# Optimization experiments

Hardware: AMD Instinct MI355X
Metric: run time of the kernel (lower is better)

The kernel has to match this reference:

```python
import math
import jax, jax.numpy as jnp
import numpy as np

DIM = 1024
FFN_DIM = 4096
NUM_HEADS = 16
HEAD_DIM = DIM // NUM_HEADS
SCALE = 1.0 / math.sqrt(HEAD_DIM)
EPS = 1e-5


def _layer_norm(x, gamma, beta):
    mu = jnp.mean(x, axis=-1, keepdims=True)
    var = jnp.mean(jnp.square(x - mu), axis=-1, keepdims=True)
    return (x - mu) * jax.lax.rsqrt(var + EPS) * gamma + beta


def _gelu_erf(x):
    # matches torch GELU module: x * 0.5 * (1 + erf(x / sqrt(2)))
    return x * 0.5 * (1.0 + jax.lax.erf(x / math.sqrt(2.0)))


def setup_inputs() -> dict:
    key = jax.random.key(0)
    ks = jax.random.split(key, 12)
    B, L = 2, 2048
    s = 0.02
    inp = {
        "x": jax.random.normal(ks[0], (B, L, DIM), dtype=jnp.float32),
        "g1": jnp.ones((DIM,), jnp.float32),
        "b1": jnp.zeros((DIM,), jnp.float32),
        "Wq": jax.random.normal(ks[1], (DIM, DIM), jnp.float32) * s,
        "bq": jnp.zeros((DIM,), jnp.float32),
        "Wk": jax.random.normal(ks[2], (DIM, DIM), jnp.float32) * s,
        "bk": jnp.zeros((DIM,), jnp.float32),
        "Wv": jax.random.normal(ks[3], (DIM, DIM), jnp.float32) * s,
        "bv": jnp.zeros((DIM,), jnp.float32),
        "Wo": jax.random.normal(ks[4], (DIM, DIM), jnp.float32) * s,
        "bo": jnp.zeros((DIM,), jnp.float32),
        "g2": jnp.ones((DIM,), jnp.float32),
        "b2": jnp.zeros((DIM,), jnp.float32),
        "W1": jax.random.normal(ks[5], (FFN_DIM, DIM), jnp.float32) * s,
        "bf1": jnp.zeros((FFN_DIM,), jnp.float32),
        "W2": jax.random.normal(ks[6], (DIM, FFN_DIM), jnp.float32) * s,
        "bf2": jnp.zeros((DIM,), jnp.float32),
    }
    return inp


def reference(x, g1, b1, Wq, bq, Wk, bk, Wv, bv, Wo, bo, g2, b2, W1, bf1, W2, bf2):
    B, L, C = x.shape
    n, c = NUM_HEADS, HEAD_DIM

    # ---- pre-norm self-attention ----
    h = _layer_norm(x, g1, b1)
    q = (h @ Wq.T + bq).reshape(B, L, n, c)
    k = (h @ Wk.T + bk).reshape(B, L, n, c)
    v = (h @ Wv.T + bv).reshape(B, L, n, c)
    attn = SCALE * jnp.einsum('binc,bjnc->bnij', q, k)   # [B, n, L, L]
    attn = jax.nn.softmax(attn, axis=-1)
    o = jnp.einsum('bnij,bjnc->binc', attn, v).reshape(B, L, C)
    x = x + (o @ Wo.T + bo)

    # ---- pre-norm FFN (GELU, erf form) ----
    h = _layer_norm(x, g2, b2)
    h = _gelu_erf(h @ W1.T + bf1)
    x = x + (h @ W2.T + bf2)
    return x
```

## Files before the change

kernel.cpp:

```cpp
#include <hip/hip_runtime.h>
#include <hip/hip_bf16.h>
#include <math.h>

typedef unsigned short u16;
typedef __attribute__((ext_vector_type(8))) __bf16 bf16x8;
typedef __attribute__((ext_vector_type(4))) float f32x4;

#define DIM   1024
#define LSEQ  2048
#define BTOK  4096
#define HD    64
#define FFN   4096
#define QSCL  0.18033688011112042f

#if __has_builtin(__builtin_amdgcn_exp2f)
#define EXP2(x) __builtin_amdgcn_exp2f(x)
#else
#define EXP2(x) exp2f(x)
#endif

__device__ __forceinline__ u16 f2bf(float f) {
  unsigned u = __builtin_bit_cast(unsigned, f);
  u += 0x7FFFu + ((u >> 16) & 1u);
  return (u16)(u >> 16);
}
__device__ __forceinline__ unsigned pk2(float a, float b) {
  return (unsigned)f2bf(a) | ((unsigned)f2bf(b) << 16);
}
__device__ __forceinline__ unsigned cvtpk(float lo, float hi) {
  unsigned r;
  asm("v_cvt_pk_bf16_f32 %0, %1, %2" : "=v"(r) : "v"(lo), "v"(hi));
  return r;
}
__device__ __forceinline__ f32x4 mfma16(bf16x8 a, bf16x8 b, f32x4 c) {
  return __builtin_amdgcn_mfma_f32_16x16x32_bf16(a, b, c, 0, 0, 0);
}
__device__ __forceinline__ void gload16(const void* g, void* l) {
  __builtin_amdgcn_global_load_lds((const __attribute__((address_space(1))) char*)g,
                                   (__attribute__((address_space(3))) char*)l, 16, 0, 0);
}
__device__ __forceinline__ float gelu_t(float v) {
  float v3 = v * v * v;
  float tt = fmaf(-0.10296766f, v3, -2.30258509f * v);
  return v * __builtin_amdgcn_rcpf(1.0f + EXP2(tt));
}

__global__ __launch_bounds__(256) void ln_kernel(const float* __restrict__ x,
                                                 const float* __restrict__ g,
                                                 const float* __restrict__ bta,
                                                 u16* __restrict__ out) {
  int row = blockIdx.x, t = threadIdx.x;
  const float* xr = x + (size_t)row * DIM;
  float4 xv = *(const float4*)(xr + t * 4);
  float s  = xv.x + xv.y + xv.z + xv.w;
  float ss = xv.x * xv.x + xv.y * xv.y + xv.z * xv.z + xv.w * xv.w;
#pragma unroll
  for (int m = 32; m >= 1; m >>= 1) {
    s  += __shfl_xor(s, m);
    ss += __shfl_xor(ss, m);
  }
  __shared__ float red[8];
  if ((t & 63) == 0) { red[(t >> 6) * 2] = s; red[(t >> 6) * 2 + 1] = ss; }
  __syncthreads();
  s  = red[0] + red[2] + red[4] + red[6];
  ss = red[1] + red[3] + red[5] + red[7];
  float mu  = s * (1.0f / DIM);
  float var = ss * (1.0f / DIM) - mu * mu;
  float rs  = rsqrtf(var + 1e-5f);
  float4 gv = *(const float4*)(g + t * 4);
  float4 bv = *(const float4*)(bta + t * 4);
  uint2 o;
  o.x = pk2((xv.x - mu) * rs * gv.x + bv.x, (xv.y - mu) * rs * gv.y + bv.y);
  o.y = pk2((xv.z - mu) * rs * gv.z + bv.z, (xv.w - mu) * rs * gv.w + bv.w);
  *(uint2*)(out + (size_t)row * DIM + t * 4) = o;
}

__global__ __launch_bounds__(256) void wcvt4(const float* __restrict__ Wq, const float* __restrict__ Wk,
                                             const float* __restrict__ Wv, const float* __restrict__ Wo,
                                             u16* __restrict__ dst) {
  int b = blockIdx.x;
  int r = b >> 9;
  const float* s = (r == 0) ? Wq : (r == 1) ? Wk : (r == 2) ? Wv : Wo;
  size_t i = (((size_t)(b & 511)) * 256 + threadIdx.x) * 8;
  float4 f0 = *(const float4*)(s + i), f1 = *(const float4*)(s + i + 4);
  uint4 o = { pk2(f0.x, f0.y), pk2(f0.z, f0.w), pk2(f1.x, f1.y), pk2(f1.z, f1.w) };
  *(uint4*)(dst + ((size_t)r << 20) + i) = o;
}
__global__ __launch_bounds__(256) void wcvt2(const float* __restrict__ W1, const float* __restrict__ W2,
                                             u16* __restrict__ d1, u16* __restrict__ d2) {
  int b = blockIdx.x;
  const float* s = (b < 2048) ? W1 : W2;
  u16* d = (b < 2048) ? d1 : d2;
  size_t i = (((size_t)(b & 2047)) * 256 + threadIdx.x) * 8;
  float4 f0 = *(const float4*)(s + i), f1 = *(const float4*)(s + i + 4);
  uint4 o = { pk2(f0.x, f0.y), pk2(f0.z, f0.w), pk2(f1.x, f1.y), pk2(f1.z, f1.w) };
  *(uint4*)(d + i) = o;
}

__global__ __launch_bounds__(256) void transpose_v(const u16* __restrict__ v,
                                                   u16* __restrict__ vt) {
  __shared__ u16 tls[64][80];
  int jb = blockIdx.x, bh = blockIdx.y, b = bh >> 4, h = bh & 15;
  int t = threadIdx.x;
  int r = t >> 2, seg = t & 3;
  const u16* src = v + (size_t)(b * LSEQ + jb * 64 + r) * DIM + h * HD + seg * 16;
  *(uint4*)&tls[r][seg * 16]     = *(const uint4*)src;
  *(uint4*)&tls[r][seg * 16 + 8] = *(const uint4*)(src + 8);
  __syncthreads();
  int c = t >> 2, jseg = t & 3;
  u16 tmp[16] __attribute__((aligned(16)));
#pragma unroll
  for (int i = 0; i < 16; i++) tmp[i] = tls[jseg * 16 + i][c];
  u16* dst = vt + ((size_t)bh * HD + c) * LSEQ + jb * 64 + jseg * 16;
  *(uint4*)dst       = *(const uint4*)tmp;
  *(uint4*)(dst + 8) = *(const uint4*)(tmp + 8);
}

__global__ __launch_bounds__(256) void prefill(float* __restrict__ io,
                                               const float* __restrict__ a,
                                               const float* __restrict__ bias) {
  size_t i = ((size_t)blockIdx.x * 256 + threadIdx.x) * 4;
  float4 va = *(const float4*)(a + i);
  float4 vc = *(const float4*)(bias + (i & (DIM - 1)));
  va.x += vc.x; va.y += vc.y; va.z += vc.z; va.w += vc.w;
  *(float4*)(io + i) = va;
}

struct GArg { const u16* Wb; const float* bias; u16* outB; float oscale; };

template <int EPI, int BM, int DEPTH>
__global__ __launch_bounds__(256) void gemm4(const u16* __restrict__ A,
                                             GArg g0, GArg g1, GArg g2,
                                             float* __restrict__ outF,
                                             int N, int Kstride, int Kiter, int nbPerW) {
  constexpr int WM  = BM / 32;
  constexpr int LPT = BM / 64 + 2;
  constexpr int ABUF = BM * 64;
  constexpr int BBUF = 8192;
  constexpr int VX  = (DEPTH - 2) * LPT;
  __shared__ u16 lsa[DEPTH][BM * 32];
  __shared__ u16 lsb[DEPTH][128 * 32];
  const int t = threadIdx.x;
  const int w = t >> 6, l = t & 63, l15 = l & 15, lg = l >> 4;
  const int wr = w >> 1, wc = w & 1;
  const int nwg = gridDim.x * gridDim.y;
  int flat = blockIdx.y * gridDim.x + blockIdx.x;
  flat = (flat & 7) * (nwg >> 3) + (flat >> 3);
  const int bx = flat % gridDim.x, by = flat / gridDim.x;
  const int sel = bx / nbPerW, nb = bx % nbPerW;
  GArg G = (sel == 0) ? g0 : ((sel == 1) ? g1 : g2);
  const int n0 = nb * 128, m0 = by * BM;
  const int z = blockIdx.z;
  const int koff = z * Kiter;

  f32x4 acc[WM][4];
#pragma unroll
  for (int m = 0; m < WM; m++)
#pragma unroll
    for (int n = 0; n < 4; n++) acc[m][n] = (f32x4){0.f, 0.f, 0.f, 0.f};

  const int grow = t >> 2;
  const int gcol = 8 * ((t & 3) ^ ((t >> 3) & 3));
  const u16* Asrc = A + (size_t)(m0 + grow) * Kstride + koff + gcol;
  const u16* Bsrc = G.Wb + (size_t)(n0 + grow) * Kstride + koff + gcol;
  const int rs = (l15 >> 1) & 3;

  const char* aadr = (const char*)lsa + (wr * (BM / 2) + l15) * 64 + (lg ^ rs) * 16;
  const char* badr = (const char*)lsb + (wc * 64 + l15) * 64 + (lg ^ rs) * 16;

  auto stage = [&](int k0, int buf) {
#pragma unroll
    for (int i = 0; i < BM / 64; i++)
      gload16(Asrc + (size_t)i * 64 * Kstride + k0, (char*)lsa + buf * ABUF + i * 4096 + w * 1024);
#pragma unroll
    for (int i = 0; i < 2; i++)
      gload16(Bsrc + (size_t)i * 64 * Kstride + k0, (char*)lsb + buf * BBUF + i * 4096 + w * 1024);
  };

#pragma unroll
  for (int p = 0; p < DEPTH - 1; p++) stage(p << 5, p);

  const int NT = Kiter >> 5;
  int bufR = 0, bufW = DEPTH - 1;
  for (int it = 0; it < NT; it++) {
    if (it + 1 < NT) {
      if constexpr (VX == 3)      asm volatile("s_waitcnt vmcnt(3)" ::: "memory");
      else if constexpr (VX == 4) asm volatile("s_waitcnt vmcnt(4)" ::: "memory");
      else if constexpr (VX == 6) asm volatile("s_waitcnt vmcnt(6)" ::: "memory");
      else                        asm volatile("s_waitcnt vmcnt(0)" ::: "memory");
    } else {
      asm volatile("s_waitcnt vmcnt(0)" ::: "memory");
    }
    __builtin_amdgcn_s_barrier();
    asm volatile("" ::: "memory");

    if (it + DEPTH - 1 < NT) stage((it + DEPTH - 1) << 5, bufW);

    const char* ap = aadr + bufR * ABUF;
    const char* bp = badr + bufR * BBUF;
    bf16x8 af[WM], bfr[4];
#pragma unroll
    for (int m = 0; m < WM; m++)
      af[m] = *(const bf16x8*)(ap + m * 1024);
#pragma unroll
    for (int n = 0; n < 4; n++)
      bfr[n] = *(const bf16x8*)(bp + n * 1024);
    __builtin_amdgcn_s_setprio(1);
#pragma unroll
    for (int m = 0; m < WM; m++)
#pragma unroll
      for (int n = 0; n < 4; n++)
        acc[m][n] = mfma16(af[m], bfr[n], acc[m][n]);
    __builtin_amdgcn_s_setprio(0);
    bufR = (bufR + 1 == DEPTH) ? 0 : bufR + 1;
    bufW = (bufW + 1 == DEPTH) ? 0 : bufW + 1;
  }

#pragma unroll
  for (int m = 0; m < WM; m++) {
    const int row = m0 + wr * (BM / 2) + m * 16 + lg * 4;
#pragma unroll
    for (int n = 0; n < 4; n++) {
      const int col = n0 + wc * 64 + n * 16 + l15;
      float bcol;
      if (EPI == 4) bcol = (z == 0 && G.bias != nullptr) ? G.bias[col] : 0.f;
      else          bcol = G.bias[col];
#pragma unroll
      for (int r = 0; r < 4; r++) {
        const float v = acc[m][n][r] + bcol;
        const size_t idx = (size_t)(row + r) * N + col;
        if (EPI == 0)      G.outB[idx] = f2bf(v * G.oscale);
        else if (EPI == 4) atomicAdd(&outF[idx], v);
        else               G.outB[idx] = f2bf(gelu_t(v));
      }
    }
  }
}

__global__ __launch_bounds__(256, 4) void attn5(const u16* __restrict__ q,
                                                const u16* __restrict__ k,
                                                const u16* __restrict__ vt,
                                                u16* __restrict__ o) {
  __shared__ __align__(16) char smem[40960];
  const int t = threadIdx.x, w = t >> 6, l = t & 63, l15 = l & 15, lg = l >> 4;
  int flat = blockIdx.y * gridDim.x + blockIdx.x;
  flat = (flat & 7) * 128 + (flat >> 3);
  const int qbk = flat & 31, bh = flat >> 5;
  const int b = bh >> 4, h = bh & 15;
  const int qrow0 = b * LSEQ + qbk * 64 + w * 16;
  const int r7 = l15 & 7;
  const int c0 = lg ^ r7;

  bf16x8 av[2];
#pragma unroll
  for (int i = 0; i < 2; i++)
    av[i] = *(const bf16x8*)(q + (size_t)(qrow0 + l15) * DIM + h * HD + i * 32 + lg * 8);

  const char* adrA  = smem + l15 * 128 + c0 * 16;
  const char* adrB  = smem + l15 * 128 + (c0 ^ 4) * 16;
  const char* padrA = smem + 32768 + w * 2048 + l15 * 128 + c0 * 16;
  const char* padrB = smem + 32768 + w * 2048 + l15 * 128 + (c0 ^ 4) * 16;
  char* pwa[4];
#pragma unroll
  for (int cb = 0; cb < 4; cb++)
    pwa[cb] = smem + 32768 + w * 2048 + l15 * 128 +
              (((2 * cb + (lg >> 1)) ^ r7) * 16) + (lg & 1) * 8;

  const int grow = t >> 3, gchk = t & 7;
  const u16* ksrc = k + (size_t)(b * LSEQ + grow) * DIM + h * HD + 8 * (gchk ^ (grow & 7));
  const u16* vsrc = vt + ((size_t)bh * HD + grow) * LSEQ + 8 * (gchk ^ (grow & 7));

  f32x4 oacc[4];
#pragma unroll
  for (int cb = 0; cb < 4; cb++) oacc[cb] = (f32x4){0.f, 0.f, 0.f, 0.f};
  f32x4 minit = (f32x4){0.f, 0.f, 0.f, 0.f};
  float lsum = 0.f;

  auto issueTile = [&](int jt, int buf) {
    const u16* kp = ksrc + (size_t)jt * DIM;
    const u16* vp = vsrc + jt;
#pragma unroll
    for (int i = 0; i < 2; i++) {
      gload16(kp + (size_t)i * 32 * DIM,  smem + buf * 8192 + i * 4096 + w * 1024);
      gload16(vp + (size_t)i * 32 * LSEQ, smem + 16384 + buf * 8192 + i * 4096 + w * 1024);
    }
  };

  issueTile(0, 0);
  for (int it = 0; it < LSEQ / 64; it++) {
    const int buf = it & 1;
    __syncthreads();
    if (it + 1 < LSEQ / 64) issueTile((it + 1) * 64, buf ^ 1);
    const int ko = buf * 8192;

    f32x4 s[4];
    const char* kA = adrA + ko;
    const char* kB = adrB + ko;
    __builtin_amdgcn_s_setprio(1);
#pragma unroll
    for (int cb = 0; cb < 4; cb++) {
      bf16x8 kf0 = *(const bf16x8*)(kA + cb * 2048);
      bf16x8 kf1 = *(const bf16x8*)(kB + cb * 2048);
      s[cb] = mfma16(kf0, av[0], minit);
      s[cb] = mfma16(kf1, av[1], s[cb]);
    }
    __builtin_amdgcn_s_setprio(0);

    float tm = fmaxf(fmaxf(fmaxf(s[0][0], s[0][1]), fmaxf(s[0][2], s[0][3])),
                     fmaxf(fmaxf(fmaxf(s[1][0], s[1][1]), fmaxf(s[1][2], s[1][3])),
                           fmaxf(fmaxf(fmaxf(s[2][0], s[2][1]), fmaxf(s[2][2], s[2][3])),
                                 fmaxf(fmaxf(s[3][0], s[3][1]), fmaxf(s[3][2], s[3][3])))));
    if (__any(tm > 8.0f)) {
      float tr = fmaxf(tm, __shfl_xor(tm, 16));
      tr = fmaxf(tr, __shfl_xor(tr, 32));
      const float d = fmaxf(tr, 0.f);
      const float scl = EXP2(-d);
      const f32x4 dv = (f32x4){d, d, d, d};
      lsum *= scl;
      minit -= dv;
#pragma unroll
      for (int cb = 0; cb < 4; cb++) s[cb] -= dv;
#pragma unroll
      for (int r = 0; r < 4; r++) {
        const float so = __shfl(scl, lg * 4 + r);
#pragma unroll
        for (int cb = 0; cb < 4; cb++) oacc[cb][r] *= so;
      }
    }
    float ps = 0.f;
    uint2 pk[4];
#pragma unroll
    for (int cb = 0; cb < 4; cb++) {
      float a0 = EXP2(s[cb][0]);
      float a1 = EXP2(s[cb][1]);
      float a2 = EXP2(s[cb][2]);
      float a3 = EXP2(s[cb][3]);
      ps += (a0 + a1) + (a2 + a3);
      pk[cb].x = cvtpk(a0, a1);
      pk[cb].y = cvtpk(a2, a3);
    }
    lsum += ps;
#pragma unroll
    for (int cb = 0; cb < 4; cb++) *(uint2*)pwa[cb] = pk[cb];

    const char* vA = adrA + ko + 16384;
    const char* vB = adrB + ko + 16384;
    bf16x8 pa0 = *(const bf16x8*)padrA;
    bf16x8 pa1 = *(const bf16x8*)padrB;
    __builtin_amdgcn_s_setprio(1);
#pragma unroll
    for (int cb = 0; cb < 4; cb++) {
      bf16x8 vf0 = *(const bf16x8*)(vA + cb * 2048);
      oacc[cb] = mfma16(pa0, vf0, oacc[cb]);
    }
#pragma unroll
    for (int cb = 0; cb < 4; cb++) {
      bf16x8 vf1 = *(const bf16x8*)(vB + cb * 2048);
      oacc[cb] = mfma16(pa1, vf1, oacc[cb]);
    }
    __builtin_amdgcn_s_setprio(0);
  }

  float rl = lsum + __shfl_xor(lsum, 16);
  rl += __shfl_xor(rl, 32);
#pragma unroll
  for (int r = 0; r < 4; r++) {
    const float lo = __shfl(rl, lg * 4 + r);
    const float rcp = 1.0f / lo;
#pragma unroll
    for (int cb = 0; cb < 4; cb++) {
      o[(size_t)(qrow0 + lg * 4 + r) * DIM + h * HD + cb * 16 + l15] =
          f2bf(oacc[cb][r] * rcp);
    }
  }
}

extern "C" void kernel_launch(void* const* d_in, const int* in_sizes, int n_in,
                              void* d_out, int out_size, void* d_ws, size_t ws_size,
                              hipStream_t stream) {
  const float* x   = (const float*)d_in[0];
  const float* g1  = (const float*)d_in[1];
  const float* b1  = (const float*)d_in[2];
  const float* Wq  = (const float*)d_in[3];
  const float* bq  = (const float*)d_in[4];
  const float* Wk  = (const float*)d_in[5];
  const float* bk  = (const float*)d_in[6];
  const float* Wv  = (const float*)d_in[7];
  const float* bv  = (const float*)d_in[8];
  const float* Wo  = (const float*)d_in[9];
  const float* bo  = (const float*)d_in[10];
  const float* g2  = (const float*)d_in[11];
  const float* b2  = (const float*)d_in[12];
  const float* W1  = (const float*)d_in[13];
  const float* bf1 = (const float*)d_in[14];
  const float* W2  = (const float*)d_in[15];
  const float* bf2 = (const float*)d_in[16];
  float* out = (float*)d_out;

  const size_t E = (size_t)BTOK * DIM;
  u16* h     = (u16*)d_ws;
  u16* qb    = h + E;
  u16* kbuf  = qb + E;
  u16* vbuf  = kbuf + E;
  u16* vtb   = vbuf + E;
  u16* wqkvo = vtb + E;
  u16* ob    = vbuf;
  u16* W1b   = qb;
  u16* W2b   = kbuf;
  u16* mid   = vbuf;
  u16* h2    = h;
  float* x2  = out;

  u16* Wqb = wqkvo;
  u16* Wkb = wqkvo + ((size_t)1 << 20);
  u16* Wvb = wqkvo + ((size_t)2 << 20);
  u16* Wob = wqkvo + ((size_t)3 << 20);

  wcvt4<<<dim3(2048), dim3(256), 0, stream>>>(Wq, Wk, Wv, Wo, wqkvo);
  ln_kernel<<<dim3(BTOK), dim3(256), 0, stream>>>(x, g1, b1, h);
  gemm4<0, 128, 3><<<dim3(24, BTOK / 128), 256, 0, stream>>>(
      h, GArg{Wqb, bq, qb, QSCL}, GArg{Wkb, bk, kbuf, 1.0f}, GArg{Wvb, bv, vbuf, 1.0f},
      nullptr, DIM, DIM, DIM, 8);
  transpose_v<<<dim3(32, 32), 256, 0, stream>>>(vbuf, vtb);
  attn5<<<dim3(LSEQ / 64, 32), 256, 0, stream>>>(qb, kbuf, vtb, ob);
  prefill<<<dim3(4096), dim3(256), 0, stream>>>(out, x, bo);
  {
    GArg s{Wob, nullptr, nullptr, 1.0f};
    gemm4<4, 128, 3><<<dim3(8, BTOK / 128, 2), 256, 0, stream>>>(
        ob, s, s, s, out, DIM, DIM, 512, 8);
  }
  wcvt2<<<dim3(4096), dim3(256), 0, stream>>>(W1, W2, W1b, W2b);
  ln_kernel<<<dim3(BTOK), dim3(256), 0, stream>>>(x2, g2, b2, h2);
  {
    GArg s{W1b, bf1, mid, 1.0f};
    gemm4<2, 128, 3><<<dim3(32, BTOK / 128), 256, 0, stream>>>(
        h2, s, s, s, nullptr, FFN, DIM, DIM, 32);
  }
  {
    GArg s{W2b, bf2, nullptr, 1.0f};
    gemm4<4, 128, 3><<<dim3(8, BTOK / 128, 2), 256, 0, stream>>>(
        mid, s, s, s, out, DIM, FFN, 2048, 8);
  }
}
```

Baseline: 285.7 us.

## Replace 128x128 GEMM with 256x256 tile, 512-thread, 4-stage kernel

Swaps the 256-thread 128x128 GEMM for a 512-thread kernel with 256x256 output tiles, 8 waves laid out 2x4, and a 4-deep LDS pipeline. Each wave now computes 128x64. All four GEMM launches move to the new kernel, and the split-K factor for the output and FFN2 projections rises from 2 to 4. The larger tile roughly doubles reuse per byte loaded and halves global traffic per flop. In exchange, LDS rises to 128 KB per block, grids shrink (e.g. 192 blocks for the QKV projection), and split-K adds more fp32 atomic traffic, which may hurt occupancy or load balance.

```diff
diff --git a/kernel.cpp b/kernel.cpp
--- a/kernel.cpp
+++ b/kernel.cpp
@@ -128,53 +128,50 @@
 
 struct GArg { const u16* Wb; const float* bias; u16* outB; float oscale; };
 
-template <int EPI, int BM, int DEPTH>
-__global__ __launch_bounds__(256) void gemm4(const u16* __restrict__ A,
-                                             GArg g0, GArg g1, GArg g2,
-                                             float* __restrict__ outF,
-                                             int N, int Kstride, int Kiter, int nbPerW) {
-  constexpr int WM  = BM / 32;
-  constexpr int LPT = BM / 64 + 2;
-  constexpr int ABUF = BM * 64;
-  constexpr int BBUF = 8192;
-  constexpr int VX  = (DEPTH - 2) * LPT;
-  __shared__ u16 lsa[DEPTH][BM * 32];
-  __shared__ u16 lsb[DEPTH][128 * 32];
+template <int EPI, int DEPTH>
+__global__ __launch_bounds__(512, 2) void gemm8(const u16* __restrict__ A,
+                                                GArg g0, GArg g1, GArg g2,
+                                                float* __restrict__ outF,
+                                                int N, int Kstride, int Kiter, int nbPerW) {
+  constexpr int BUFB = 16384;
+  constexpr int VX   = (DEPTH - 2) * 4;
+  __shared__ u16 lsa[DEPTH][256 * 32];
+  __shared__ u16 lsb[DEPTH][256 * 32];
   const int t = threadIdx.x;
   const int w = t >> 6, l = t & 63, l15 = l & 15, lg = l >> 4;
-  const int wr = w >> 1, wc = w & 1;
+  const int wr = w >> 2, wc = w & 3;
   const int nwg = gridDim.x * gridDim.y;
   int flat = blockIdx.y * gridDim.x + blockIdx.x;
   flat = (flat & 7) * (nwg >> 3) + (flat >> 3);
   const int bx = flat % gridDim.x, by = flat / gridDim.x;
   const int sel = bx / nbPerW, nb = bx % nbPerW;
   GArg G = (sel == 0) ? g0 : ((sel == 1) ? g1 : g2);
-  const int n0 = nb * 128, m0 = by * BM;
+  const int n0 = nb * 256, m0 = by * 256;
   const int z = blockIdx.z;
   const int koff = z * Kiter;
 
-  f32x4 acc[WM][4];
-#pragma unroll
-  for (int m = 0; m < WM; m++)
+  f32x4 acc[8][4];
+#pragma unroll
+  for (int m = 0; m < 8; m++)
 #pragma unroll
     for (int n = 0; n < 4; n++) acc[m][n] = (f32x4){0.f, 0.f, 0.f, 0.f};
 
-  const int grow = t >> 2;
-  const int gcol = 8 * ((t & 3) ^ ((t >> 3) & 3));
-  const u16* Asrc = A + (size_t)(m0 + grow) * Kstride + koff + gcol;
-  const u16* Bsrc = G.Wb + (size_t)(n0 + grow) * Kstride + koff + gcol;
+  const int srow = l >> 2;
+  const int scol = 8 * ((l & 3) ^ ((l >> 3) & 3));
+  const u16* AsrcT = A    + (size_t)(m0 + w * 32 + srow) * Kstride + koff + scol;
+  const u16* BsrcT = G.Wb + (size_t)(n0 + w * 32 + srow) * Kstride + koff + scol;
+
   const int rs = (l15 >> 1) & 3;
-
-  const char* aadr = (const char*)lsa + (wr * (BM / 2) + l15) * 64 + (lg ^ rs) * 16;
-  const char* badr = (const char*)lsb + (wc * 64 + l15) * 64 + (lg ^ rs) * 16;
+  const char* aadr = (const char*)lsa + (wr * 128 + l15) * 64 + ((lg ^ rs) * 16);
+  const char* badr = (const char*)lsb + (wc * 64  + l15) * 64 + ((lg ^ rs) * 16);
 
   auto stage = [&](int k0, int buf) {
 #pragma unroll
-    for (int i = 0; i < BM / 64; i++)
-      gload16(Asrc + (size_t)i * 64 * Kstride + k0, (char*)lsa + buf * ABUF + i * 4096 + w * 1024);
-#pragma unroll
-    for (int i = 0; i < 2; i++)
-      gload16(Bsrc + (size_t)i * 64 * Kstride + k0, (char*)lsb + buf * BBUF + i * 4096 + w * 1024);
+    for (int j = 0; j < 2; j++)
+      gload16(AsrcT + (size_t)j * 16 * Kstride + k0, (char*)lsa + buf * BUFB + (w * 2 + j) * 1024);
+#pragma unroll
+    for (int j = 0; j < 2; j++)
+      gload16(BsrcT + (size_t)j * 16 * Kstride + k0, (char*)lsb + buf * BUFB + (w * 2 + j) * 1024);
   };
 
 #pragma unroll
@@ -184,9 +181,8 @@
   int bufR = 0, bufW = DEPTH - 1;
   for (int it = 0; it < NT; it++) {
     if (it + 1 < NT) {
-      if constexpr (VX == 3)      asm volatile("s_waitcnt vmcnt(3)" ::: "memory");
-      else if constexpr (VX == 4) asm volatile("s_waitcnt vmcnt(4)" ::: "memory");
-      else if constexpr (VX == 6) asm volatile("s_waitcnt vmcnt(6)" ::: "memory");
+      if constexpr (VX == 4)      asm volatile("s_waitcnt vmcnt(4)" ::: "memory");
+      else if constexpr (VX == 8) asm volatile("s_waitcnt vmcnt(8)" ::: "memory");
       else                        asm volatile("s_waitcnt vmcnt(0)" ::: "memory");
     } else {
       asm volatile("s_waitcnt vmcnt(0)" ::: "memory");
@@ -196,29 +192,28 @@
 
     if (it + DEPTH - 1 < NT) stage((it + DEPTH - 1) << 5, bufW);
 
-    const char* ap = aadr + bufR * ABUF;
-    const char* bp = badr + bufR * BBUF;
-    bf16x8 af[WM], bfr[4];
-#pragma unroll
-    for (int m = 0; m < WM; m++)
-      af[m] = *(const bf16x8*)(ap + m * 1024);
+    const char* ap = aadr + bufR * BUFB;
+    const char* bp = badr + bufR * BUFB;
+    bf16x8 bfr[4];
 #pragma unroll
     for (int n = 0; n < 4; n++)
       bfr[n] = *(const bf16x8*)(bp + n * 1024);
     __builtin_amdgcn_s_setprio(1);
 #pragma unroll
-    for (int m = 0; m < WM; m++)
+    for (int m = 0; m < 8; m++) {
+      bf16x8 af = *(const bf16x8*)(ap + m * 1024);
 #pragma unroll
       for (int n = 0; n < 4; n++)
-        acc[m][n] = mfma16(af[m], bfr[n], acc[m][n]);
+        acc[m][n] = mfma16(af, bfr[n], acc[m][n]);
+    }
     __builtin_amdgcn_s_setprio(0);
     bufR = (bufR + 1 == DEPTH) ? 0 : bufR + 1;
     bufW = (bufW + 1 == DEPTH) ? 0 : bufW + 1;
   }
 
 #pragma unroll
-  for (int m = 0; m < WM; m++) {
-    const int row = m0 + wr * (BM / 2) + m * 16 + lg * 4;
+  for (int m = 0; m < 8; m++) {
+    const int row = m0 + wr * 128 + m * 16 + lg * 4;
 #pragma unroll
     for (int n = 0; n < 4; n++) {
       const int col = n0 + wc * 64 + n * 16 + l15;
@@ -418,27 +413,27 @@
 
   wcvt4<<<dim3(2048), dim3(256), 0, stream>>>(Wq, Wk, Wv, Wo, wqkvo);
   ln_kernel<<<dim3(BTOK), dim3(256), 0, stream>>>(x, g1, b1, h);
-  gemm4<0, 128, 3><<<dim3(24, BTOK / 128), 256, 0, stream>>>(
+  gemm8<0, 4><<<dim3(12, BTOK / 256), 512, 0, stream>>>(
       h, GArg{Wqb, bq, qb, QSCL}, GArg{Wkb, bk, kbuf, 1.0f}, GArg{Wvb, bv, vbuf, 1.0f},
-      nullptr, DIM, DIM, DIM, 8);
+      nullptr, DIM, DIM, DIM, 4);
   transpose_v<<<dim3(32, 32), 256, 0, stream>>>(vbuf, vtb);
   attn5<<<dim3(LSEQ / 64, 32), 256, 0, stream>>>(qb, kbuf, vtb, ob);
   prefill<<<dim3(4096), dim3(256), 0, stream>>>(out, x, bo);
   {
     GArg s{Wob, nullptr, nullptr, 1.0f};
-    gemm4<4, 128, 3><<<dim3(8, BTOK / 128, 2), 256, 0, stream>>>(
-        ob, s, s, s, out, DIM, DIM, 512, 8);
+    gemm8<4, 4><<<dim3(4, BTOK / 256, 4), 512, 0, stream>>>(
+        ob, s, s, s, out, DIM, DIM, 256, 4);
   }
   wcvt2<<<dim3(4096), dim3(256), 0, stream>>>(W1, W2, W1b, W2b);
   ln_kernel<<<dim3(BTOK), dim3(256), 0, stream>>>(x2, g2, b2, h2);
   {
     GArg s{W1b, bf1, mid, 1.0f};
-    gemm4<2, 128, 3><<<dim3(32, BTOK / 128), 256, 0, stream>>>(
-        h2, s, s, s, nullptr, FFN, DIM, DIM, 32);
+    gemm8<2, 4><<<dim3(16, BTOK / 256), 512, 0, stream>>>(
+        h2, s, s, s, nullptr, FFN, DIM, DIM, 16);
   }
   {
     GArg s{W2b, bf2, nullptr, 1.0f};
-    gemm4<4, 128, 3><<<dim3(8, BTOK / 128, 2), 256, 0, stream>>>(
-        mid, s, s, s, out, DIM, FFN, 2048, 8);
-  }
-}
+    gemm8<4, 4><<<dim3(4, BTOK / 256, 4), 512, 0, stream>>>(
+        mid, s, s, s, out, DIM, FFN, 1024, 4);
+  }
+}
```

New measurement: 331.1 us. +15.9%, slower.
